# Performance work log

Hardware: AMD Instinct MI355X
Metric: run time of the kernel (lower is better)

Reference implementation:

```python
import jax, jax.numpy as jnp
import numpy as np

D_MODEL = 256
D_STATE = 64
D_CONV = 4
EXPAND = 2
HEADDIM = 64
D_INNER = EXPAND * D_MODEL            # 512
NHEADS = D_INNER // HEADDIM           # 8
CONV_DIM = D_INNER + 2 * D_STATE      # 640 (ngroups=1)
BATCH = 8
SEQ = 4096


def setup_inputs() -> dict:
    key = jax.random.key(0)
    ks = jax.random.split(key, 6)
    x = jax.random.normal(ks[0], (BATCH, SEQ, D_MODEL), jnp.float32)
    d_in_proj = 2 * D_INNER + 2 * D_STATE + NHEADS  # 1160
    W_in = jax.random.normal(ks[1], (d_in_proj, D_MODEL), jnp.float32) / np.sqrt(D_MODEL)
    conv_w = jax.random.normal(ks[2], (CONV_DIM, D_CONV), jnp.float32) / np.sqrt(D_CONV)
    conv_b = jnp.zeros((CONV_DIM,), jnp.float32)
    # dt_bias = inverse-softplus of dt sampled log-uniform in [1e-3, 0.1] (mamba_ssm init)
    dt = jnp.exp(jax.random.uniform(ks[3], (NHEADS,), jnp.float32, np.log(1e-3), np.log(0.1)))
    dt_bias = dt + jnp.log(-jnp.expm1(-dt))
    A_log = jnp.log(jax.random.uniform(ks[4], (NHEADS,), jnp.float32, 1.0, 16.0))
    Dp = jnp.ones((NHEADS,), jnp.float32)
    gnorm_w = jnp.ones((D_INNER,), jnp.float32)
    norm_w = jnp.ones((D_MODEL,), jnp.float32)
    W_out = jax.random.normal(ks[5], (D_MODEL, D_INNER), jnp.float32) / np.sqrt(D_INNER)
    return {"x": x, "W_in": W_in, "conv_w": conv_w, "conv_b": conv_b,
            "dt_bias": dt_bias, "A_log": A_log, "Dp": Dp,
            "gnorm_w": gnorm_w, "norm_w": norm_w, "W_out": W_out}


def _rmsnorm(x, w, eps):
    return x * jax.lax.rsqrt(jnp.mean(x * x, axis=-1, keepdims=True) + eps) * w


def reference(x, W_in, conv_w, conv_b, dt_bias, A_log, Dp, gnorm_w, norm_w, W_out):
    Bsz, L, _ = x.shape
    # pre-norm (torch nn.RMSNorm eps=None -> finfo eps)
    xn = _rmsnorm(x, norm_w, jnp.finfo(x.dtype).eps)
    zxbcdt = jnp.einsum('bld,ed->ble', xn, W_in)            # (B,L,1160)
    z = zxbcdt[..., :D_INNER]                               # gate (B,L,512)
    xBC = zxbcdt[..., D_INNER:D_INNER + CONV_DIM]           # (B,L,640)
    dt = zxbcdt[..., -NHEADS:]                              # (B,L,8)
    # causal depthwise conv1d + silu
    xpad = jnp.pad(xBC, ((0, 0), (D_CONV - 1, 0), (0, 0)))
    conv = sum(xpad[:, k:k + L, :] * conv_w[:, k] for k in range(D_CONV)) + conv_b
    xBC = jax.nn.silu(conv)
    xs = xBC[..., :D_INNER].reshape(Bsz, L, NHEADS, HEADDIM)  # (B,L,H,P)
    Bm = xBC[..., D_INNER:D_INNER + D_STATE]                  # (B,L,N)
    Cm = xBC[..., D_INNER + D_STATE:]                         # (B,L,N)
    dt = jax.nn.softplus(dt + dt_bias)                        # (B,L,H)
    dA = jnp.exp(dt * (-jnp.exp(A_log)))                      # (B,L,H)

    def step(state, inp):
        dA_t, dt_t, B_t, C_t, x_t = inp  # (B,H) (B,H) (B,N) (B,N) (B,H,P)
        state = state * dA_t[:, :, None, None] \
            + (dt_t[:, :, None] * x_t)[..., None] * B_t[:, None, None, :]
        y = jnp.einsum('bhpn,bn->bhp', state, C_t)
        return state, y

    init = jnp.zeros((Bsz, NHEADS, HEADDIM, D_STATE), x.dtype)
    tm = lambda a: jnp.moveaxis(a, 1, 0)  # time-major for scan
    _, ys = jax.lax.scan(step, init, (tm(dA), tm(dt), tm(Bm), tm(Cm), tm(xs)))
    y = jnp.moveaxis(ys, 0, 1) + Dp[None, None, :, None] * xs  # skip D term
    y = y.reshape(Bsz, L, D_INNER)
    # gated RMSNorm (norm_before_gate=False): rmsnorm(y * silu(z))
    y = _rmsnorm(y * jax.nn.silu(z), gnorm_w, 1e-5)
    return x + jnp.einsum('ble,de->bld', y, W_out)
```

## Files before the change

### kernel.cpp

```cpp
#include <hip/hip_runtime.h>
#include <math.h>

#define BATCH   8
#define SEQ     4096
#define DMODEL  256
#define DINNER  512
#define DSTATE  64
#define NHEADS  8
#define HEADDIM 64
#define CONVDIM 640
#define DPROJ   1160
#define ZSTR    1152
#define NROWS   (BATCH*SEQ)
#define CHUNK   64
#define NCHUNK  (SEQ/CHUNK)
#define LSTR    72

typedef short bf16x8 __attribute__((ext_vector_type(8)));
typedef short short8v __attribute__((ext_vector_type(8)));
typedef float f32x4 __attribute__((ext_vector_type(4)));

__device__ short g_xn[(size_t)NROWS * DMODEL];
__device__ short g_zxb[(size_t)NROWS * ZSTR];
__device__ short g_xbc[(size_t)NROWS * CONVDIM];
__device__ float g_dt[(size_t)NROWS * NHEADS];
__device__ float g_rowss[(size_t)NROWS * NHEADS];
__device__ short g_lstate[(size_t)BATCH * NHEADS * NCHUNK * HEADDIM * DSTATE];
__device__ float g_decayC[BATCH * NHEADS * NCHUNK];
__device__ short g_Winb[(size_t)ZSTR * DMODEL];
__device__ short g_Woutb[(size_t)DMODEL * DINNER];

__device__ __forceinline__ short f2bf(float f) {
    unsigned u = __float_as_uint(f);
    u += 0x7fff + ((u >> 16) & 1);
    return (short)(u >> 16);
}
__device__ __forceinline__ float bf2f(short s) {
    return __uint_as_float(((unsigned)(unsigned short)s) << 16);
}

__device__ __forceinline__ void stage16(const void* gsrc, void* ldst) {
    __builtin_amdgcn_global_load_lds(
        (const __attribute__((address_space(1))) void*)gsrc,
        (__attribute__((address_space(3))) void*)ldst, 16, 0, 0);
}

__device__ __forceinline__ int swz(int row, int col) {
    return row * 64 + ((((col >> 3) ^ row) & 7) << 3) + (col & 7);
}

__global__ __launch_bounds__(256) void convert_bf16_kernel(const float* __restrict__ src,
                                                           short* __restrict__ dst,
                                                           int n_valid, int n_total) {
    const int i = blockIdx.x * 256 + threadIdx.x;
    if (i < n_total) dst[i] = (i < n_valid) ? f2bf(src[i]) : (short)0;
}

__global__ __launch_bounds__(256) void convert_wout_kernel(const float* __restrict__ src,
                                                           const float* __restrict__ gw,
                                                           short* __restrict__ dst) {
    const int i = blockIdx.x * 256 + threadIdx.x;
    if (i < DMODEL * DINNER) dst[i] = f2bf(src[i] * gw[i % DINNER]);
}

__global__ __launch_bounds__(256) void rmsnorm_dt_kernel(const float* __restrict__ x,
                                                         const float* __restrict__ w,
                                                         const float* __restrict__ W_in,
                                                         short* __restrict__ xn,
                                                         float* __restrict__ dt) {
    const int row  = blockIdx.x * 4 + (threadIdx.x >> 6);
    const int lane = threadIdx.x & 63;
    const float4 v = *(const float4*)(x + (size_t)row * DMODEL + lane * 4);
    float ss = v.x * v.x + v.y * v.y + v.z * v.z + v.w * v.w;
#pragma unroll
    for (int off = 1; off < 64; off <<= 1) ss += __shfl_xor(ss, off);
    const float rs = rsqrtf(ss * (1.0f / DMODEL) + 1.1920929e-7f);
    const float4 wv = *(const float4*)(w + lane * 4);
    const float4 xn4 = make_float4(v.x * rs * wv.x, v.y * rs * wv.y,
                                   v.z * rs * wv.z, v.w * rs * wv.w);
    short4 o;
    o.x = f2bf(xn4.x); o.y = f2bf(xn4.y); o.z = f2bf(xn4.z); o.w = f2bf(xn4.w);
    *(short4*)(xn + (size_t)row * DMODEL + lane * 4) = o;
#pragma unroll
    for (int h = 0; h < NHEADS; ++h) {
        const float4 ww = *(const float4*)(W_in + (size_t)(DPROJ - NHEADS + h) * DMODEL + lane * 4);
        float p = xn4.x * ww.x + xn4.y * ww.y + xn4.z * ww.z + xn4.w * ww.w;
#pragma unroll
        for (int off = 1; off < 64; off <<= 1) p += __shfl_xor(p, off);
        if (lane == 0) dt[(size_t)row * NHEADS + h] = p;
    }
}

template <bool RES, typename OUT>
__global__ __launch_bounds__(256) void gemm_bf16_nt(const short* __restrict__ A,
                                                    const short* __restrict__ B,
                                                    const float* __restrict__ R,
                                                    const float* __restrict__ RS,
                                                    OUT* __restrict__ C,
                                                    int NX, int M, int N, int K, int LDA) {
    const int L   = blockIdx.x;
    const int xcd = L & 7;
    const int r   = L >> 3;
    const int mstrips_per_xcd = (M / 128) >> 3;
    const int mblk = xcd * mstrips_per_xcd + r / NX;
    const int nblk = r % NX;
    const int m0 = mblk * 128, n0 = nblk * 128;

    __shared__ __align__(16) short Asl[128 * 64];
    __shared__ __align__(16) short Bsl[128 * 64];
    const int tid  = threadIdx.x;
    const int lane = tid & 63;
    const int wid  = tid >> 6;
    const int wrow = (wid >> 1) * 64, wcol = (wid & 1) * 64;

    f32x4 acc[4][4];
#pragma unroll
    for (int m = 0; m < 4; ++m)
#pragma unroll
        for (int n = 0; n < 4; ++n) acc[m][n] = (f32x4)0.f;

    const int wbase = (tid & 0xC0) * 8;

    for (int k0 = 0; k0 < K; k0 += 64) {
#pragma unroll
        for (int rr = 0; rr < 4; ++rr) {
            const int idx = rr * 256 + tid;
            const int row = idx >> 3;
            const int cs  = idx & 7;
            const int ko  = (cs ^ (row & 7)) * 8;
            const int r6  = row & 63;
            const int brow = (row & 64) + (((r6 & 15) << 2) | (r6 >> 4));
            stage16(A + (size_t)(m0 + row) * LDA + k0 + ko, Asl + rr * 2048 + wbase);
            stage16(B + (size_t)(n0 + brow) * K + k0 + ko, Bsl + rr * 2048 + wbase);
        }
        __syncthreads();
#pragma unroll
        for (int ks = 0; ks < 2; ++ks) {
            bf16x8 af[4], bfr[4];
#pragma unroll
            for (int m = 0; m < 4; ++m) {
                const int arow = wrow + m * 16 + (lane & 15);
                const int ch = (ks * 4 + (lane >> 4)) ^ (arow & 7);
                af[m] = *(const bf16x8*)(Asl + arow * 64 + ch * 8);
            }
#pragma unroll
            for (int n = 0; n < 4; ++n) {
                const int brw = wcol + n * 16 + (lane & 15);
                const int ch = (ks * 4 + (lane >> 4)) ^ (brw & 7);
                bfr[n] = *(const bf16x8*)(Bsl + brw * 64 + ch * 8);
            }
#pragma unroll
            for (int m = 0; m < 4; ++m)
#pragma unroll
                for (int n = 0; n < 4; ++n)
                    acc[m][n] = __builtin_amdgcn_mfma_f32_16x16x32_bf16(af[m], bfr[n], acc[m][n], 0, 0, 0);
        }
        __syncthreads();
    }

    const int r0 = (lane >> 4) * 4;
    const int gcol = n0 + wcol + (lane & 15) * 4;
#pragma unroll
    for (int m = 0; m < 4; ++m) {
        const int grow = m0 + wrow + m * 16 + r0;
        if (gcol < N) {
#pragma unroll
            for (int reg = 0; reg < 4; ++reg) {
                if constexpr (sizeof(OUT) == 2) {
                    short4 o;
                    o.x = f2bf(acc[m][0][reg]); o.y = f2bf(acc[m][1][reg]);
                    o.z = f2bf(acc[m][2][reg]); o.w = f2bf(acc[m][3][reg]);
                    *(short4*)(C + (size_t)(grow + reg) * N + gcol) = o;
                } else {
                    f32x4 v;
                    v[0] = acc[m][0][reg]; v[1] = acc[m][1][reg];
                    v[2] = acc[m][2][reg]; v[3] = acc[m][3][reg];
                    if (RES) {
                        const float* rp = RS + (size_t)(grow + reg) * NHEADS;
                        const f32x4 s0 = *(const f32x4*)rp;
                        const f32x4 s1 = *(const f32x4*)(rp + 4);
                        const float sum = s0[0] + s0[1] + s0[2] + s0[3] +
                                          s1[0] + s1[1] + s1[2] + s1[3];
                        const float rsn = rsqrtf(sum * (1.0f / DINNER) + 1e-5f);
                        v *= rsn;
                        v += *(const f32x4*)(R + (size_t)(grow + reg) * N + gcol);
                    }
                    *(f32x4*)(C + (size_t)(grow + reg) * N + gcol) = v;
                }
            }
        }
    }
}

__global__ __launch_bounds__(256) void conv_silu_kernel(const short* __restrict__ zxb,
                                                        const float* __restrict__ cw,
                                                        const float* __restrict__ cb,
                                                        short* __restrict__ xbc) {
    const int idx = blockIdx.x * 256 + threadIdx.x;
    const int c8  = (idx % 80) * 8;
    const int bl0 = (idx / 80) * 8;
    const int l0  = bl0 & (SEQ - 1);
    const short* src = zxb + (size_t)bl0 * ZSTR + DINNER + c8;

    float4 w4[8];
    float bias[8];
#pragma unroll
    for (int j = 0; j < 8; ++j) w4[j] = *(const float4*)(cw + (c8 + j) * 4);
    {
        const float4 b0 = *(const float4*)(cb + c8);
        const float4 b1 = *(const float4*)(cb + c8 + 4);
        bias[0] = b0.x; bias[1] = b0.y; bias[2] = b0.z; bias[3] = b0.w;
        bias[4] = b1.x; bias[5] = b1.y; bias[6] = b1.z; bias[7] = b1.w;
    }

    bf16x8 rowv[11];
#pragma unroll
    for (int m = 0; m < 11; ++m) {
        if (l0 + m - 3 >= 0)
            rowv[m] = *(const bf16x8*)(src + (ptrdiff_t)(m - 3) * ZSTR);
        else
            rowv[m] = (bf16x8)0;
    }

#pragma unroll
    for (int r = 0; r < 8; ++r) {
        float acc[8];
#pragma unroll
        for (int j = 0; j < 8; ++j) acc[j] = bias[j];
#pragma unroll
        for (int k = 0; k < 4; ++k) {
            const bf16x8 tap = rowv[r + k];
#pragma unroll
            for (int j = 0; j < 8; ++j)
                acc[j] = fmaf(bf2f(tap[j]), ((const float*)&w4[j])[k], acc[j]);
        }
        short8v o;
#pragma unroll
        for (int j = 0; j < 8; ++j) {
            const float s = acc[j];
            o[j] = f2bf(s / (1.f + __expf(-s)));
        }
        *(short8v*)(xbc + (size_t)(bl0 + r) * CONVDIM + c8) = o;
    }
}

__global__ __launch_bounds__(256) void chunk_state_mfma(const float* __restrict__ dt,
                                                        const short* __restrict__ xbc,
                                                        const float* __restrict__ dt_bias,
                                                        const float* __restrict__ A_log,
                                                        short* __restrict__ lstate,
                                                        float* __restrict__ decayC) {
    const int bhc = blockIdx.x;
    const int c = bhc & (NCHUNK - 1), bh = bhc >> 6, h = bh & (NHEADS - 1), b = bh >> 3;
    const int tid = threadIdx.x, lane = tid & 63, wid = tid >> 6;
    __shared__ short XT[64 * LSTR];
    __shared__ short BT[64 * LSTR];
    __shared__ float wsh[CHUNK];
    const size_t row0 = (size_t)b * SEQ + (size_t)c * CHUNK;

    const float aneg  = -__expf(A_log[h]);
    const float dbias = dt_bias[h];
    if (tid < 64) {
        const float draw = dt[(row0 + tid) * NHEADS + h] + dbias;
        const float dtv  = (draw > 20.f) ? draw : log1pf(__expf(draw));
        float cum = aneg * dtv;
#pragma unroll
        for (int off = 1; off < 64; off <<= 1) {
            const float nv = __shfl_up(cum, off);
            if (lane >= off) cum += nv;
        }
        const float total = __shfl(cum, 63);
        wsh[tid] = __expf(total - cum) * dtv;
        if (tid == 63) decayC[bhc] = __expf(cum);
    }
    __syncthreads();

#pragma unroll
    for (int r = 0; r < 4; ++r) {
        const int idx  = tid + r * 256;
        const int trow = idx >> 4;
        const int q    = idx & 15;
        const int c4   = q * 4;
        const short* rp = xbc + (row0 + trow) * CONVDIM;
        const short4 xv = *(const short4*)(rp + h * 64 + c4);
        const short4 bv = *(const short4*)(rp + DINNER + c4);
        const float w = wsh[trow];
        XT[(0 * 16 + q) * LSTR + trow] = xv.x;
        XT[(1 * 16 + q) * LSTR + trow] = xv.y;
        XT[(2 * 16 + q) * LSTR + trow] = xv.z;
        XT[(3 * 16 + q) * LSTR + trow] = xv.w;
        BT[(0 * 16 + q) * LSTR + trow] = f2bf(bf2f(bv.x) * w);
        BT[(1 * 16 + q) * LSTR + trow] = f2bf(bf2f(bv.y) * w);
        BT[(2 * 16 + q) * LSTR + trow] = f2bf(bf2f(bv.z) * w);
        BT[(3 * 16 + q) * LSTR + trow] = f2bf(bf2f(bv.w) * w);
    }
    __syncthreads();

    f32x4 acc[4];
#pragma unroll
    for (int n = 0; n < 4; ++n) acc[n] = (f32x4)0.f;
#pragma unroll
    for (int ks = 0; ks < 2; ++ks) {
        const bf16x8 af = *(const bf16x8*)(XT + (wid * 16 + (lane & 15)) * LSTR + ks * 32 + (lane >> 4) * 8);
#pragma unroll
        for (int n = 0; n < 4; ++n) {
            const bf16x8 bfv = *(const bf16x8*)(BT + (n * 16 + (lane & 15)) * LSTR + ks * 32 + (lane >> 4) * 8);
            acc[n] = __builtin_amdgcn_mfma_f32_16x16x32_bf16(af, bfv, acc[n], 0, 0, 0);
        }
    }
    short* lp = lstate + ((size_t)bhc << 12);
    const int hi = lane >> 4;
    const int ncol = (lane & 15) * 4;
#pragma unroll
    for (int reg = 0; reg < 4; ++reg) {
        const int p = 16 * hi + 4 * reg + wid;
        short4 o;
        o.x = f2bf(acc[0][reg]); o.y = f2bf(acc[1][reg]);
        o.z = f2bf(acc[2][reg]); o.w = f2bf(acc[3][reg]);
        *(short4*)(lp + p * 64 + ncol) = o;
    }
}

__global__ __launch_bounds__(256) void state_prefix_kernel(short* __restrict__ lstate,
                                                           const float* __restrict__ decayC) {
    const int idx = blockIdx.x * 256 + threadIdx.x;
    const int bh  = idx >> 10;
    const int pn4 = (idx & 1023) * 4;
    float S0 = 0.f, S1 = 0.f, S2 = 0.f, S3 = 0.f;
    for (int c = 0; c < NCHUNK; ++c) {
        short4* ptr = (short4*)(lstate + (((size_t)bh * NCHUNK + c) << 12) + pn4);
        const short4 l4 = *ptr;
        short4 o;
        o.x = f2bf(S0); o.y = f2bf(S1); o.z = f2bf(S2); o.w = f2bf(S3);
        *ptr = o;
        const float d = decayC[bh * NCHUNK + c];
        S0 = fmaf(S0, d, bf2f(l4.x));
        S1 = fmaf(S1, d, bf2f(l4.y));
        S2 = fmaf(S2, d, bf2f(l4.z));
        S3 = fmaf(S3, d, bf2f(l4.w));
    }
}

__global__ __launch_bounds__(256) void chunk_scan_mfma(const float* __restrict__ dt,
                                                       short* __restrict__ xbc,
                                                       const short* __restrict__ zxb,
                                                       float* __restrict__ rowss,
                                                       const float* __restrict__ dt_bias,
                                                       const float* __restrict__ A_log,
                                                       const float* __restrict__ Dp,
                                                       const short* __restrict__ lstate) {
    const int bhc = blockIdx.x;
    const int c = bhc & (NCHUNK - 1), bh = bhc >> 6, h = bh & (NHEADS - 1), b = bh >> 3;
    const int tid = threadIdx.x, lane = tid & 63, wid = tid >> 6;
    __shared__ short BsMs[64 * 64];
    __shared__ short Cs[64 * 64];
    __shared__ short XT[64 * 64];
    __shared__ short SP[64 * 64];
    short* Bs = BsMs;
    short* Ms = BsMs;
    const size_t row0 = (size_t)b * SEQ + (size_t)c * CHUNK;

    const float aneg  = -__expf(A_log[h]);
    const float dbias = dt_bias[h];
    const float draw = dt[(row0 + lane) * NHEADS + h] + dbias;
    const float dtv  = (draw > 20.f) ? draw : log1pf(__expf(draw));
    float cum = aneg * dtv;
#pragma unroll
    for (int off = 1; off < 64; off <<= 1) {
        const float nv = __shfl_up(cum, off);
        if (lane >= off) cum += nv;
    }

#pragma unroll
    for (int r = 0; r < 4; ++r) {
        const int idx  = tid + r * 256;
        const int trow = idx >> 4;
        const int q    = idx & 15;
        const int c4   = q * 4;
        const short* rp = xbc + (row0 + trow) * CONVDIM;
        const short4 xv = *(const short4*)(rp + h * 64 + c4);
        const int hoff = ((((q >> 1) ^ trow) & 7) << 3) + (q & 1) * 4;
        *(short4*)(Bs + trow * 64 + hoff) = *(const short4*)(rp + DINNER + c4);
        *(short4*)(Cs + trow * 64 + hoff) = *(const short4*)(rp + DINNER + DSTATE + c4);
        XT[swz(0 * 16 + q, trow)] = xv.x;
        XT[swz(1 * 16 + q, trow)] = xv.y;
        XT[swz(2 * 16 + q, trow)] = xv.z;
        XT[swz(3 * 16 + q, trow)] = xv.w;
    }
#pragma unroll
    for (int r = 0; r < 4; ++r) {
        const int idx = tid + r * 256;
        const int p = idx >> 4, q = idx & 15;
        const int pslot = ((p & 3) << 4) | (p >> 2);
        const int hoff = ((((q >> 1) ^ pslot) & 7) << 3) + (q & 1) * 4;
        *(short4*)(SP + pslot * 64 + hoff) =
            *(const short4*)(lstate + ((size_t)bhc << 12) + p * 64 + q * 4);
    }
    __syncthreads();

    f32x4 accG[4];
#pragma unroll
    for (int tf = 0; tf < 4; ++tf) accG[tf] = (f32x4)0.f;
    __builtin_amdgcn_s_setprio(1);
#pragma unroll
    for (int ks = 0; ks < 2; ++ks) {
        const int crow = wid * 16 + (lane & 15);
        const bf16x8 af = *(const bf16x8*)(Cs + crow * 64 + (((ks * 4 + (lane >> 4)) ^ crow) & 7) * 8);
#pragma unroll
        for (int tf = 0; tf < 4; ++tf) {
            const int brw = tf * 16 + (lane & 15);
            const bf16x8 bfv = *(const bf16x8*)(Bs + brw * 64 + (((ks * 4 + (lane >> 4)) ^ brw) & 7) * 8);
            accG[tf] = __builtin_amdgcn_mfma_f32_16x16x32_bf16(af, bfv, accG[tf], 0, 0, 0);
        }
    }
    __builtin_amdgcn_s_setprio(0);
    __syncthreads();

    const int srow0 = wid * 16 + (lane >> 4) * 4;
    float csr[4];
#pragma unroll
    for (int reg = 0; reg < 4; ++reg) csr[reg] = __shfl(cum, srow0 + reg);
#pragma unroll
    for (int tf = 0; tf < 4; ++tf) {
        const int t = tf * 16 + (lane & 15);
        const float ct  = __shfl(cum, t);
        const float dtt = __shfl(dtv, t);
#pragma unroll
        for (int reg = 0; reg < 4; ++reg) {
            const int s = srow0 + reg;
            const float m = (t <= s) ? accG[tf][reg] * __expf(csr[reg] - ct) * dtt : 0.f;
            Ms[swz(s, t)] = f2bf(m);
        }
    }
    __syncthreads();

    f32x4 acc1[4], acc2[4];
#pragma unroll
    for (int pf = 0; pf < 4; ++pf) { acc1[pf] = (f32x4)0.f; acc2[pf] = (f32x4)0.f; }
    __builtin_amdgcn_s_setprio(1);
#pragma unroll
    for (int ks = 0; ks < 2; ++ks) {
        const int mrow = wid * 16 + (lane & 15);
        const int ch = ks * 4 + (lane >> 4);
        const bf16x8 am = *(const bf16x8*)(Ms + mrow * 64 + ((ch ^ mrow) & 7) * 8);
        const bf16x8 ac = *(const bf16x8*)(Cs + mrow * 64 + ((ch ^ mrow) & 7) * 8);
#pragma unroll
        for (int pf = 0; pf < 4; ++pf) {
            const int prow = pf * 16 + (lane & 15);
            const bf16x8 bx = *(const bf16x8*)(XT + prow * 64 + ((ch ^ prow) & 7) * 8);
            const bf16x8 bs = *(const bf16x8*)(SP + prow * 64 + ((ch ^ prow) & 7) * 8);
            acc1[pf] = __builtin_amdgcn_mfma_f32_16x16x32_bf16(am, bx, acc1[pf], 0, 0, 0);
            acc2[pf] = __builtin_amdgcn_mfma_f32_16x16x32_bf16(ac, bs, acc2[pf], 0, 0, 0);
        }
    }
    __builtin_amdgcn_s_setprio(0);
    const float dpv = Dp[h];
    float es[4];
#pragma unroll
    for (int reg = 0; reg < 4; ++reg) es[reg] = __expf(csr[reg]);
    const int j = lane & 15;
#pragma unroll
    for (int reg = 0; reg < 4; ++reg) {
        const int s = srow0 + reg;
        const short4 z4 = *(const short4*)(zxb + (row0 + s) * ZSTR + h * 64 + j * 4);
        short4 o;
        float ssq = 0.f;
#pragma unroll
        for (int pf = 0; pf < 4; ++pf) {
            const float xv = bf2f(XT[swz(pf * 16 + j, s)]);
            const float yv = acc1[pf][reg] + es[reg] * acc2[pf][reg] + dpv * xv;
            const float zf = bf2f(((const short*)&z4)[pf]);
            const float v  = yv * zf / (1.f + __expf(-zf));
            ((short*)&o)[pf] = f2bf(v);
            ssq = fmaf(v, v, ssq);
        }
        *(short4*)(xbc + (row0 + s) * CONVDIM + h * 64 + j * 4) = o;
        ssq += __shfl_xor(ssq, 1);
        ssq += __shfl_xor(ssq, 2);
        ssq += __shfl_xor(ssq, 4);
        ssq += __shfl_xor(ssq, 8);
        if (j == 0) rowss[(row0 + s) * NHEADS + h] = ssq;
    }
}

extern "C" void kernel_launch(void* const* d_in, const int* in_sizes, int n_in,
                              void* d_out, int out_size, void* d_ws, size_t ws_size,
                              hipStream_t stream) {
    (void)in_sizes; (void)n_in; (void)out_size; (void)d_ws; (void)ws_size;
    const float* x      = (const float*)d_in[0];
    const float* W_in   = (const float*)d_in[1];
    const float* conv_w = (const float*)d_in[2];
    const float* conv_b = (const float*)d_in[3];
    const float* dt_b   = (const float*)d_in[4];
    const float* A_log  = (const float*)d_in[5];
    const float* Dp     = (const float*)d_in[6];
    const float* g_w    = (const float*)d_in[7];
    const float* n_w    = (const float*)d_in[8];
    const float* W_out  = (const float*)d_in[9];
    float* out = (float*)d_out;

    short *xn, *zxb, *xbc, *winb, *woutb, *lst;
    float *dtv, *dcy, *rss;
    hipGetSymbolAddress((void**)&xn,    HIP_SYMBOL(g_xn));
    hipGetSymbolAddress((void**)&zxb,   HIP_SYMBOL(g_zxb));
    hipGetSymbolAddress((void**)&xbc,   HIP_SYMBOL(g_xbc));
    hipGetSymbolAddress((void**)&dtv,   HIP_SYMBOL(g_dt));
    hipGetSymbolAddress((void**)&rss,   HIP_SYMBOL(g_rowss));
    hipGetSymbolAddress((void**)&lst,   HIP_SYMBOL(g_lstate));
    hipGetSymbolAddress((void**)&dcy,   HIP_SYMBOL(g_decayC));
    hipGetSymbolAddress((void**)&winb,  HIP_SYMBOL(g_Winb));
    hipGetSymbolAddress((void**)&woutb, HIP_SYMBOL(g_Woutb));

    convert_bf16_kernel<<<(ZSTR * DMODEL) / 256, 256, 0, stream>>>(
        W_in, winb, ZSTR * DMODEL, ZSTR * DMODEL);
    convert_wout_kernel<<<(DMODEL * DINNER) / 256, 256, 0, stream>>>(W_out, g_w, woutb);

    rmsnorm_dt_kernel<<<NROWS / 4, 256, 0, stream>>>(x, n_w, W_in, xn, dtv);

    gemm_bf16_nt<false, short><<<(ZSTR / 128) * (NROWS / 128), 256, 0, stream>>>(
        xn, winb, nullptr, nullptr, zxb, ZSTR / 128, NROWS, ZSTR, DMODEL, DMODEL);

    conv_silu_kernel<<<(NROWS / 8 * 80) / 256, 256, 0, stream>>>(zxb, conv_w, conv_b, xbc);

    chunk_state_mfma<<<BATCH * NHEADS * NCHUNK, 256, 0, stream>>>(dtv, xbc, dt_b, A_log, lst, dcy);
    state_prefix_kernel<<<(BATCH * NHEADS * HEADDIM * DSTATE) / (4 * 256), 256, 0, stream>>>(lst, dcy);
    chunk_scan_mfma<<<BATCH * NHEADS * NCHUNK, 256, 0, stream>>>(
        dtv, xbc, zxb, rss, dt_b, A_log, Dp, lst);

    gemm_bf16_nt<true, float><<<(DMODEL / 128) * (NROWS / 128), 256, 0, stream>>>(
        xbc, woutb, x, rss, out, DMODEL / 128, NROWS, DMODEL, DINNER, CONVDIM);
}
```

Before: 173.2 us.

## Share chunk C·Bᵀ Gram matrix across four heads per chunk_scan block

Each chunk_scan block now handles a chunk for a group of four heads instead of a single head. The B and C loads and the C·Bᵀ Gram MFMA, which are identical for every head because there is only one group, are done once and kept in registers, then reused for each head in a loop. This removes redundant global loads of B/C and repeated Gram matmuls. In exchange the grid is four times smaller and each block runs a serialized loop with extra barriers, which lowers parallelism and latency hiding.

After: 184.4 us. 1.06x slower.

```diff
diff --git a/kernel.cpp b/kernel.cpp
--- a/kernel.cpp
+++ b/kernel.cpp
@@ -349,8 +349,11 @@
                                                        const float* __restrict__ A_log,
                                                        const float* __restrict__ Dp,
                                                        const short* __restrict__ lstate) {
-    const int bhc = blockIdx.x;
-    const int c = bhc & (NCHUNK - 1), bh = bhc >> 6, h = bh & (NHEADS - 1), b = bh >> 3;
+    const int bid = blockIdx.x;
+    const int c   = bid & (NCHUNK - 1);
+    const int rest = bid >> 6;
+    const int hg  = rest & 1;
+    const int b   = rest >> 1;
     const int tid = threadIdx.x, lane = tid & 63, wid = tid >> 6;
     __shared__ short BsMs[64 * 64];
     __shared__ short Cs[64 * 64];
@@ -360,17 +363,6 @@
     short* Ms = BsMs;
     const size_t row0 = (size_t)b * SEQ + (size_t)c * CHUNK;
 
-    const float aneg  = -__expf(A_log[h]);
-    const float dbias = dt_bias[h];
-    const float draw = dt[(row0 + lane) * NHEADS + h] + dbias;
-    const float dtv  = (draw > 20.f) ? draw : log1pf(__expf(draw));
-    float cum = aneg * dtv;
-#pragma unroll
-    for (int off = 1; off < 64; off <<= 1) {
-        const float nv = __shfl_up(cum, off);
-        if (lane >= off) cum += nv;
-    }
-
 #pragma unroll
     for (int r = 0; r < 4; ++r) {
         const int idx  = tid + r * 256;
@@ -378,23 +370,9 @@
         const int q    = idx & 15;
         const int c4   = q * 4;
         const short* rp = xbc + (row0 + trow) * CONVDIM;
-        const short4 xv = *(const short4*)(rp + h * 64 + c4);
         const int hoff = ((((q >> 1) ^ trow) & 7) << 3) + (q & 1) * 4;
         *(short4*)(Bs + trow * 64 + hoff) = *(const short4*)(rp + DINNER + c4);
         *(short4*)(Cs + trow * 64 + hoff) = *(const short4*)(rp + DINNER + DSTATE + c4);
-        XT[swz(0 * 16 + q, trow)] = xv.x;
-        XT[swz(1 * 16 + q, trow)] = xv.y;
-        XT[swz(2 * 16 + q, trow)] = xv.z;
-        XT[swz(3 * 16 + q, trow)] = xv.w;
-    }
-#pragma unroll
-    for (int r = 0; r < 4; ++r) {
-        const int idx = tid + r * 256;
-        const int p = idx >> 4, q = idx & 15;
-        const int pslot = ((p & 3) << 4) | (p >> 2);
-        const int hoff = ((((q >> 1) ^ pslot) & 7) << 3) + (q & 1) * 4;
-        *(short4*)(SP + pslot * 64 + hoff) =
-            *(const short4*)(lstate + ((size_t)bhc << 12) + p * 64 + q * 4);
     }
     __syncthreads();
 
@@ -414,72 +392,111 @@
         }
     }
     __builtin_amdgcn_s_setprio(0);
-    __syncthreads();
 
     const int srow0 = wid * 16 + (lane >> 4) * 4;
-    float csr[4];
-#pragma unroll
-    for (int reg = 0; reg < 4; ++reg) csr[reg] = __shfl(cum, srow0 + reg);
-#pragma unroll
-    for (int tf = 0; tf < 4; ++tf) {
-        const int t = tf * 16 + (lane & 15);
-        const float ct  = __shfl(cum, t);
-        const float dtt = __shfl(dtv, t);
+    const int j = lane & 15;
+
+    for (int hh = 0; hh < 4; ++hh) {
+        const int h = hg * 4 + hh;
+        __syncthreads();
+
+#pragma unroll
+        for (int r = 0; r < 4; ++r) {
+            const int idx  = tid + r * 256;
+            const int trow = idx >> 4;
+            const int q    = idx & 15;
+            const int c4   = q * 4;
+            const short4 xv = *(const short4*)(xbc + (row0 + trow) * CONVDIM + h * 64 + c4);
+            XT[swz(0 * 16 + q, trow)] = xv.x;
+            XT[swz(1 * 16 + q, trow)] = xv.y;
+            XT[swz(2 * 16 + q, trow)] = xv.z;
+            XT[swz(3 * 16 + q, trow)] = xv.w;
+        }
+        const size_t lbase = ((size_t)(((b * NHEADS) + h) * NCHUNK + c)) << 12;
+#pragma unroll
+        for (int r = 0; r < 4; ++r) {
+            const int idx = tid + r * 256;
+            const int p = idx >> 4, q = idx & 15;
+            const int pslot = ((p & 3) << 4) | (p >> 2);
+            const int hoff = ((((q >> 1) ^ pslot) & 7) << 3) + (q & 1) * 4;
+            *(short4*)(SP + pslot * 64 + hoff) =
+                *(const short4*)(lstate + lbase + p * 64 + q * 4);
+        }
+
+        const float aneg = -__expf(A_log[h]);
+        const float draw = dt[(row0 + lane) * NHEADS + h] + dt_bias[h];
+        const float dtv  = (draw > 20.f) ? draw : log1pf(__expf(draw));
+        float cum = aneg * dtv;
+#pragma unroll
+        for (int off = 1; off < 64; off <<= 1) {
+            const float nv = __shfl_up(cum, off);
+            if (lane >= off) cum += nv;
+        }
+        float csr[4];
+#pragma unroll
+        for (int reg = 0; reg < 4; ++reg) csr[reg] = __shfl(cum, srow0 + reg);
+
+#pragma unroll
+        for (int tf = 0; tf < 4; ++tf) {
+            const int t = tf * 16 + j;
+            const float ct  = __shfl(cum, t);
+            const float dtt = __shfl(dtv, t);
+#pragma unroll
+            for (int reg = 0; reg < 4; ++reg) {
+                const int s = srow0 + reg;
+                const float m = (t <= s) ? accG[tf][reg] * __expf(csr[reg] - ct) * dtt : 0.f;
+                Ms[swz(s, t)] = f2bf(m);
+            }
+        }
+        __syncthreads();
+
+        f32x4 acc1[4], acc2[4];
+#pragma unroll
+        for (int pf = 0; pf < 4; ++pf) { acc1[pf] = (f32x4)0.f; acc2[pf] = (f32x4)0.f; }
+        __builtin_amdgcn_s_setprio(1);
+#pragma unroll
+        for (int ks = 0; ks < 2; ++ks) {
+            const int mrow = wid * 16 + j;
+            const int ch = ks * 4 + (lane >> 4);
+            const bf16x8 am = *(const bf16x8*)(Ms + mrow * 64 + ((ch ^ mrow) & 7) * 8);
+            const bf16x8 ac = *(const bf16x8*)(Cs + mrow * 64 + ((ch ^ mrow) & 7) * 8);
+#pragma unroll
+            for (int pf = 0; pf < 4; ++pf) {
+                const int prow = pf * 16 + j;
+                const bf16x8 bx = *(const bf16x8*)(XT + prow * 64 + ((ch ^ prow) & 7) * 8);
+                const bf16x8 bs = *(const bf16x8*)(SP + prow * 64 + ((ch ^ prow) & 7) * 8);
+                acc1[pf] = __builtin_amdgcn_mfma_f32_16x16x32_bf16(am, bx, acc1[pf], 0, 0, 0);
+                acc2[pf] = __builtin_amdgcn_mfma_f32_16x16x32_bf16(ac, bs, acc2[pf], 0, 0, 0);
+            }
+        }
+        __builtin_amdgcn_s_setprio(0);
+
+        const float dpv = Dp[h];
+        float es[4];
+#pragma unroll
+        for (int reg = 0; reg < 4; ++reg) es[reg] = __expf(csr[reg]);
 #pragma unroll
         for (int reg = 0; reg < 4; ++reg) {
             const int s = srow0 + reg;
-            const float m = (t <= s) ? accG[tf][reg] * __expf(csr[reg] - ct) * dtt : 0.f;
-            Ms[swz(s, t)] = f2bf(m);
-        }
-    }
-    __syncthreads();
-
-    f32x4 acc1[4], acc2[4];
-#pragma unroll
-    for (int pf = 0; pf < 4; ++pf) { acc1[pf] = (f32x4)0.f; acc2[pf] = (f32x4)0.f; }
-    __builtin_amdgcn_s_setprio(1);
-#pragma unroll
-    for (int ks = 0; ks < 2; ++ks) {
-        const int mrow = wid * 16 + (lane & 15);
-        const int ch = ks * 4 + (lane >> 4);
-        const bf16x8 am = *(const bf16x8*)(Ms + mrow * 64 + ((ch ^ mrow) & 7) * 8);
-        const bf16x8 ac = *(const bf16x8*)(Cs + mrow * 64 + ((ch ^ mrow) & 7) * 8);
-#pragma unroll
-        for (int pf = 0; pf < 4; ++pf) {
-            const int prow = pf * 16 + (lane & 15);
-            const bf16x8 bx = *(const bf16x8*)(XT + prow * 64 + ((ch ^ prow) & 7) * 8);
-            const bf16x8 bs = *(const bf16x8*)(SP + prow * 64 + ((ch ^ prow) & 7) * 8);
-            acc1[pf] = __builtin_amdgcn_mfma_f32_16x16x32_bf16(am, bx, acc1[pf], 0, 0, 0);
-            acc2[pf] = __builtin_amdgcn_mfma_f32_16x16x32_bf16(ac, bs, acc2[pf], 0, 0, 0);
-        }
-    }
-    __builtin_amdgcn_s_setprio(0);
-    const float dpv = Dp[h];
-    float es[4];
-#pragma unroll
-    for (int reg = 0; reg < 4; ++reg) es[reg] = __expf(csr[reg]);
-    const int j = lane & 15;
-#pragma unroll
-    for (int reg = 0; reg < 4; ++reg) {
-        const int s = srow0 + reg;
-        const short4 z4 = *(const short4*)(zxb + (row0 + s) * ZSTR + h * 64 + j * 4);
-        short4 o;
-        float ssq = 0.f;
-#pragma unroll
-        for (int pf = 0; pf < 4; ++pf) {
-            const float xv = bf2f(XT[swz(pf * 16 + j, s)]);
-            const float yv = acc1[pf][reg] + es[reg] * acc2[pf][reg] + dpv * xv;
-            const float zf = bf2f(((const short*)&z4)[pf]);
-            const float v  = yv * zf / (1.f + __expf(-zf));
-            ((short*)&o)[pf] = f2bf(v);
-            ssq = fmaf(v, v, ssq);
-        }
-        *(short4*)(xbc + (row0 + s) * CONVDIM + h * 64 + j * 4) = o;
-        ssq += __shfl_xor(ssq, 1);
-        ssq += __shfl_xor(ssq, 2);
-        ssq += __shfl_xor(ssq, 4);
-        ssq += __shfl_xor(ssq, 8);
-        if (j == 0) rowss[(row0 + s) * NHEADS + h] = ssq;
+            const short4 z4 = *(const short4*)(zxb + (row0 + s) * ZSTR + h * 64 + j * 4);
+            short4 o;
+            float ssq = 0.f;
+#pragma unroll
+            for (int pf = 0; pf < 4; ++pf) {
+                const float xv = bf2f(XT[swz(pf * 16 + j, s)]);
+                const float yv = acc1[pf][reg] + es[reg] * acc2[pf][reg] + dpv * xv;
+                const float zf = bf2f(((const short*)&z4)[pf]);
+                const float v  = yv * zf / (1.f + __expf(-zf));
+                ((short*)&o)[pf] = f2bf(v);
+                ssq = fmaf(v, v, ssq);
+            }
+            *(short4*)(xbc + (row0 + s) * CONVDIM + h * 64 + j * 4) = o;
+            ssq += __shfl_xor(ssq, 1);
+            ssq += __shfl_xor(ssq, 2);
+            ssq += __shfl_xor(ssq, 4);
+            ssq += __shfl_xor(ssq, 8);
+            if (j == 0) rowss[(row0 + s) * NHEADS + h] = ssq;
+        }
     }
 }
 
@@ -524,7 +541,7 @@
 
     chunk_state_mfma<<<BATCH * NHEADS * NCHUNK, 256, 0, stream>>>(dtv, xbc, dt_b, A_log, lst, dcy);
     state_prefix_kernel<<<(BATCH * NHEADS * HEADDIM * DSTATE) / (4 * 256), 256, 0, stream>>>(lst, dcy);
-    chunk_scan_mfma<<<BATCH * NHEADS * NCHUNK, 256, 0, stream>>>(
+    chunk_scan_mfma<<<BATCH * 2 * NCHUNK, 256, 0, stream>>>(
         dtv, xbc, zxb, rss, dt_b, A_log, Dp, lst);
 
     gemm_bf16_nt<true, float><<<(DMODEL / 128) * (NROWS / 128), 256, 0, stream>>>(
```
